# Performance work log

Hardware: AMD Instinct MI355X
Metric: run time of the kernel (lower is better)

Reference implementation:

```python
import jax, jax.numpy as jnp
import numpy as np

B, S, D, H, F, M = 4, 2048, 1024, 16, 4096, 1024
HD = D // H
EPS = 1e-6


def _rms(x, scale):
    # flax nn.RMSNorm: x * rsqrt(mean(x^2) + eps) * scale
    return x * jax.lax.rsqrt(jnp.mean(x * x, axis=-1, keepdims=True) + EPS) * scale


def setup_inputs() -> dict:
    key = jax.random.key(0)
    ks = jax.random.split(key, 40)
    w = lambda k, shape: jax.random.normal(k, shape, jnp.float32) * 0.02
    inp = {
        'x': jax.random.normal(ks[0], (B, S, D), jnp.float32),
        'mem_k': jax.random.normal(ks[1], (B, M, D), jnp.float32),
        'mem_v': jax.random.normal(ks[2], (B, M, D), jnp.float32),
        'n1': jnp.ones((D,), jnp.float32),
        'n2': jnp.ones((D,), jnp.float32),
        'wq': w(ks[3], (D, D)), 'bq': jnp.zeros((D,), jnp.float32),
        'wk': w(ks[4], (D, D)), 'bk': jnp.zeros((D,), jnp.float32),
        'wv': w(ks[5], (D, D)), 'bv': jnp.zeros((D,), jnp.float32),
        'wz': w(ks[6], (D, D)), 'bz': jnp.zeros((D,), jnp.float32),
        'wgz': w(ks[7], (D, D)), 'bgz': jnp.zeros((D,), jnp.float32),
        'wgh': w(ks[8], (D, D)), 'bgh': jnp.zeros((D,), jnp.float32),
        'wg1': w(ks[9], (D, D // 4)), 'bg1': jnp.zeros((D // 4,), jnp.float32),
        'wg2': w(ks[10], (D // 4, D)), 'bg2': jnp.full((D,), -3.0, jnp.float32),
        'wc1': w(ks[11], (D, D // 4)), 'bc1': jnp.zeros((D // 4,), jnp.float32),
        'wc2': w(ks[12], (D // 4, D)), 'bc2': jnp.zeros((D,), jnp.float32),
        'wak': w(ks[13], (D, D)), 'bak': jnp.zeros((D,), jnp.float32),
        'wav': w(ks[14], (D, D)), 'bav': jnp.zeros((D,), jnp.float32),
        'wao': w(ks[15], (D, D)), 'bao': jnp.zeros((D,), jnp.float32),
        'w1': w(ks[16], (D, F)), 'b1': jnp.zeros((F,), jnp.float32),
        'w2': w(ks[17], (F, D)), 'b2': jnp.zeros((D,), jnp.float32),
    }
    return inp


def reference(x, mem_k, mem_v, n1, n2, wq, bq, wk, bk, wv, bv, wz, bz,
              wgz, bgz, wgh, bgh, wg1, bg1, wg2, bg2, wc1, bc1, wc2, bc2,
              wak, bak, wav, bav, wao, bao, w1, b1, w2, b2):
    x_norm = _rms(x, n1)
    q = x_norm @ wq + bq
    k = x_norm @ wk + bk
    v = x_norm @ wv + bv
    z = x_norm @ wz + bz

    # decay gamma: base from z, context modulation from k
    gamma_base = jax.nn.sigmoid(jax.nn.gelu(x_norm @ wz @ jnp.zeros((0,)) if False else (z @ wg1 + bg1)) @ wg2 + bg2)
    gamma_mod = jax.nn.sigmoid(jax.nn.gelu(k @ wc1 + bc1) @ wc2 + bc2)
    gamma = jnp.clip(gamma_base * gamma_mod, 1e-6, 1.0 - 1e-6)

    gate_z_seq = z @ wgz + bgz
    h0 = jnp.zeros((x.shape[0], D), x.dtype)

    def scan_fn(h_prev, inputs):
        gz_t, z_t, g_t = inputs  # each [B, D]
        gate = jax.nn.sigmoid(gz_t + h_prev @ wgh + bgh)
        h_tilde = (1.0 - gate) * h_prev + gate * z_t
        h_t = jnp.clip(h_tilde + g_t * h_prev, -100.0, 100.0)
        return h_t, h_t

    xs = (jnp.swapaxes(gate_z_seq, 0, 1), jnp.swapaxes(z, 0, 1), jnp.swapaxes(gamma, 0, 1))
    _, h_seq_T = jax.lax.scan(scan_fn, h0, xs)  # [S, B, D]
    h_sequence = jnp.swapaxes(h_seq_T, 0, 1)  # [B, S, D]

    # MultiMemoryAttention: queries from q_input, keys/values from memory state
    qh = q.reshape(B, S, H, HD)
    kh = (mem_k @ wak + bak).reshape(B, M, H, HD)
    vh = (mem_v @ wav + bav).reshape(B, M, H, HD)
    scores = jnp.einsum('bqhd,bkhd->bhqk', qh, kh) / jnp.sqrt(jnp.float32(HD))
    attn = jax.nn.softmax(scores, axis=-1)
    mem_out = jnp.einsum('bhqk,bkhd->bqhd', attn, vh).reshape(B, S, D) @ wao + bao

    combined = h_sequence + mem_out + v * 0.1
    x_residual = x + combined  # dropout deterministic
    x_norm2 = _rms(x_residual, n2)
    h_ffn = jax.nn.gelu(x_norm2 @ w1 + b1) @ w2 + b2
    return x_residual + h_ffn
```

## Files before the change

kernel.cpp:

```cpp
#include <hip/hip_runtime.h>

namespace {

constexpr int kB = 4, kS = 2048, kD = 1024, kH = 16, kF = 4096, kM = 1024;
constexpr int kBS = kB * kS;
constexpr int kBM = kB * kM;

#define DEV __device__ __forceinline__

DEV float bf2f(unsigned short u){ unsigned int i = ((unsigned int)u) << 16; float f; __builtin_memcpy(&f, &i, 4); return f; }
DEV unsigned short f2bf(float f){ unsigned int i; __builtin_memcpy(&i, &f, 4); return (unsigned short)((i + 0x7fffu + ((i >> 16) & 1u)) >> 16); }
DEV float gelu_f(float x){ float u = 0.7978845608028654f * (x + 0.044715f * x * x * x); return 0.5f * x * (1.0f + tanhf(u)); }
DEV float sigmoid_f(float x){ return 1.0f / (1.0f + __expf(-x)); }

typedef __attribute__((ext_vector_type(8))) short bf16x8;
typedef __attribute__((ext_vector_type(4))) float f32x4;
typedef __attribute__((address_space(1))) const unsigned char gas_u8;
typedef __attribute__((address_space(3))) unsigned char las_u8;

__global__ __launch_bounds__(256) void k_transpose_bf16(const float* __restrict__ W, unsigned short* __restrict__ Wt, int K, int N){
  __shared__ float tile[32][33];
  int n0 = blockIdx.x * 32, k0 = blockIdx.y * 32;
  int tx = threadIdx.x, ty = threadIdx.y;
  for (int i = ty; i < 32; i += 8) tile[i][tx] = W[(size_t)(k0 + i) * N + n0 + tx];
  __syncthreads();
  for (int i = ty; i < 32; i += 8) Wt[(size_t)(n0 + i) * K + k0 + tx] = f2bf(tile[tx][i]);
}

__global__ __launch_bounds__(256) void k_rmsnorm(const float* __restrict__ x, const float* __restrict__ scale, unsigned short* __restrict__ out){
  int row = blockIdx.x;
  int t = threadIdx.x;
  float4 v = ((const float4*)(x + (size_t)row * kD))[t];
  float ss = v.x*v.x + v.y*v.y + v.z*v.z + v.w*v.w;
  for (int o = 32; o > 0; o >>= 1) ss += __shfl_xor(ss, o);
  __shared__ float red[4];
  int wave = t >> 6, lane = t & 63;
  if (lane == 0) red[wave] = ss;
  __syncthreads();
  float tot = red[0] + red[1] + red[2] + red[3];
  float r = rsqrtf(tot * (1.0f / kD) + 1e-6f);
  float4 s = ((const float4*)scale)[t];
  ushort4 o4;
  o4.x = f2bf(v.x * r * s.x); o4.y = f2bf(v.y * r * s.y);
  o4.z = f2bf(v.z * r * s.z); o4.w = f2bf(v.w * r * s.w);
  *(ushort4*)(out + (size_t)row * kD + t * 4) = o4;
}

__global__ __launch_bounds__(256) void k_f32_to_bf16(const float* __restrict__ in, unsigned short* __restrict__ out, int n4){
  int i = blockIdx.x * 256 + threadIdx.x;
  int stride = gridDim.x * 256;
  for (; i < n4; i += stride){
    float4 v = ((const float4*)in)[i];
    ushort4 o; o.x = f2bf(v.x); o.y = f2bf(v.y); o.z = f2bf(v.z); o.w = f2bf(v.w);
    ((ushort4*)out)[i] = o;
  }
}

__global__ __launch_bounds__(256) void k_combine(float* __restrict__ xres, const float* __restrict__ x,
                                                 const float* __restrict__ h, const unsigned short* __restrict__ v, int n4){
  int i = blockIdx.x * 256 + threadIdx.x;
  int stride = gridDim.x * 256;
  for (; i < n4; i += stride){
    float4 a = ((float4*)xres)[i];
    float4 xv = ((const float4*)x)[i];
    float4 hv = ((const float4*)h)[i];
    ushort4 vv = ((const ushort4*)v)[i];
    a.x += xv.x + hv.x + 0.1f * bf2f(vv.x);
    a.y += xv.y + hv.y + 0.1f * bf2f(vv.y);
    a.z += xv.z + hv.z + 0.1f * bf2f(vv.z);
    a.w += xv.w + hv.w + 0.1f * bf2f(vv.w);
    ((float4*)xres)[i] = a;
  }
}

template<int EPI>
__global__ __launch_bounds__(256) void gemm_kernel(
    const unsigned short* __restrict__ A, int lda,
    const unsigned short* __restrict__ Bt, int ldb,
    const float* __restrict__ bias,
    float* __restrict__ out1, unsigned short* __restrict__ out2,
    const float* __restrict__ src,
    int Mdim, int Ndim, int Kdim,
    const float* __restrict__ b_k = nullptr,
    const float* __restrict__ b_v = nullptr,
    const float* __restrict__ b_z = nullptr,
    unsigned short* __restrict__ o_k = nullptr,
    unsigned short* __restrict__ o_v = nullptr,
    unsigned short* __restrict__ o_zb = nullptr)
{
  __shared__ unsigned short As[128 * 32];
  __shared__ unsigned short Bs[128 * 32];
  const int t = threadIdx.x;
  const int wave = t >> 6, lane = t & 63;
  const int m0 = blockIdx.y * 128, n0 = blockIdx.x * 128;
  const int wr = (wave >> 1) * 64, wc = (wave & 1) * 64;
  const int lr = lane & 15, lk = lane >> 4;

  f32x4 acc[4][4];
  #pragma unroll
  for (int m = 0; m < 4; ++m)
    #pragma unroll
    for (int n = 0; n < 4; ++n) acc[m][n] = (f32x4){0.f, 0.f, 0.f, 0.f};

  const int r0 = t >> 2, s0 = (t & 3) * 8;
  const int r1 = 64 + r0;
  las_u8* lA0 = (las_u8*)(void*)(As + r0 * 32 + s0);
  las_u8* lA1 = (las_u8*)(void*)(As + r1 * 32 + s0);
  las_u8* lB0 = (las_u8*)(void*)(Bs + r0 * 32 + s0);
  las_u8* lB1 = (las_u8*)(void*)(Bs + r1 * 32 + s0);

  for (int k0 = 0; k0 < Kdim; k0 += 32){
    __syncthreads();
    __builtin_amdgcn_global_load_lds((gas_u8*)(const void*)(A  + (size_t)(m0 + r0) * lda + k0 + s0), lA0, 16, 0, 0);
    __builtin_amdgcn_global_load_lds((gas_u8*)(const void*)(A  + (size_t)(m0 + r1) * lda + k0 + s0), lA1, 16, 0, 0);
    __builtin_amdgcn_global_load_lds((gas_u8*)(const void*)(Bt + (size_t)(n0 + r0) * ldb + k0 + s0), lB0, 16, 0, 0);
    __builtin_amdgcn_global_load_lds((gas_u8*)(const void*)(Bt + (size_t)(n0 + r1) * ldb + k0 + s0), lB1, 16, 0, 0);
    __syncthreads();
    bf16x8 af[4], bfr[4];
    #pragma unroll
    for (int m = 0; m < 4; ++m) af[m] = *(const bf16x8*)(As + (wr + m * 16 + lr) * 32 + lk * 8);
    #pragma unroll
    for (int n = 0; n < 4; ++n) bfr[n] = *(const bf16x8*)(Bs + (wc + n * 16 + lr) * 32 + lk * 8);
    #pragma unroll
    for (int m = 0; m < 4; ++m)
      #pragma unroll
      for (int n = 0; n < 4; ++n)
        acc[m][n] = __builtin_amdgcn_mfma_f32_16x16x32_bf16(af[m], bfr[n], acc[m][n], 0, 0, 0);
  }

  const float* bsel = bias;
  unsigned short* osel = out2;
  int sel = 0;
  if constexpr (EPI == 8){
    sel = n0 >> 10;
    bsel = (sel == 0) ? bias : (sel == 1) ? b_k : (sel == 2) ? b_v : b_z;
    osel = (sel == 0) ? out2 : (sel == 1) ? o_k : (sel == 2) ? o_v : o_zb;
  }

  #pragma unroll
  for (int m = 0; m < 4; ++m){
    #pragma unroll
    for (int n = 0; n < 4; ++n){
      int col = n0 + wc + n * 16 + lr;
      float bv;
      if constexpr (EPI == 8) bv = bsel[col & 1023];
      else bv = bias ? bias[col] : 0.f;
      #pragma unroll
      for (int r = 0; r < 4; ++r){
        int rowg = m0 + wr + m * 16 + lk * 4 + r;
        size_t off = (size_t)rowg * Ndim + col;
        float v = acc[m][n][r] + bv;
        if constexpr (EPI == 0) out1[off] = v;
        else if constexpr (EPI == 1) out2[off] = f2bf(v);
        else if constexpr (EPI == 2) out2[off] = f2bf(gelu_f(v));
        else if constexpr (EPI == 3) out1[off] = sigmoid_f(v);
        else if constexpr (EPI == 4){ float g = out1[off] * sigmoid_f(v); out1[off] = fminf(fmaxf(g, 1e-6f), 1.0f - 1e-6f); }
        else if constexpr (EPI == 5){ out1[off] = v; out2[off] = f2bf(v); }
        else if constexpr (EPI == 6) out1[off] = src[off] + v;
        else if constexpr (EPI == 7) out1[off] += v;
        else if constexpr (EPI == 8){
          size_t off8 = (size_t)rowg * 1024 + (col & 1023);
          if (sel == 3){ out1[off8] = v; osel[off8] = f2bf(v); }
          else osel[off8] = f2bf(v);
        }
        else if constexpr (EPI == 9){
          int bb = rowg >> 10, key = rowg & 1023, hh = col >> 6, dd = col & 63;
          out2[(((size_t)bb * 16 + hh) * 64 + dd) * 1024 + key] = f2bf(v);
        }
      }
    }
  }
}

__global__ __launch_bounds__(256) void k_scan(const float* __restrict__ wgh,
                                              const float* __restrict__ gz,
                                              float* __restrict__ zh ,
                                              const float* __restrict__ gamma,
                                              const float* __restrict__ bgh,
                                              unsigned long long* __restrict__ hpub){
  __shared__ unsigned short wsl[1024 * 32];
  __shared__ float hl[1024];
  __shared__ float red[4][32];
  const int t = threadIdx.x;
  const int bid = blockIdx.x;
  const int b = bid & 3, slc = bid >> 2;
  const int colg0 = slc * 32;

  for (int idx = t; idx < 32768; idx += 256){
    int k = idx >> 5, c = idx & 31;
    wsl[idx] = f2bf(wgh[(size_t)k * 1024 + colg0 + c]);
  }
  const float bghv = (t < 32) ? bgh[colg0 + t] : 0.f;
  const int lane = t & 63, w = t >> 6;
  const int lgrp = lane >> 3;
  const int lcol = lane & 7;
  const int ibase = w * 256;
  __syncthreads();

  for (int tt = 0; tt < kS; ++tt){
    if (tt > 0){
      const unsigned want = (unsigned)(tt - 1);
      unsigned long long* pb = hpub + (((size_t)((tt - 1) & 1)) * kB + b) * 1024 + ibase + (lane << 2);
      unsigned long long pv0 = __hip_atomic_load(pb + 0, __ATOMIC_RELAXED, __HIP_MEMORY_SCOPE_AGENT);
      unsigned long long pv1 = __hip_atomic_load(pb + 1, __ATOMIC_RELAXED, __HIP_MEMORY_SCOPE_AGENT);
      unsigned long long pv2 = __hip_atomic_load(pb + 2, __ATOMIC_RELAXED, __HIP_MEMORY_SCOPE_AGENT);
      unsigned long long pv3 = __hip_atomic_load(pb + 3, __ATOMIC_RELAXED, __HIP_MEMORY_SCOPE_AGENT);
      while (true){
        bool ok = ((unsigned)(pv0 >> 32) == want) && ((unsigned)(pv1 >> 32) == want)
               && ((unsigned)(pv2 >> 32) == want) && ((unsigned)(pv3 >> 32) == want);
        if (__all(ok)) break;
        pv0 = __hip_atomic_load(pb + 0, __ATOMIC_RELAXED, __HIP_MEMORY_SCOPE_AGENT);
        pv1 = __hip_atomic_load(pb + 1, __ATOMIC_RELAXED, __HIP_MEMORY_SCOPE_AGENT);
        pv2 = __hip_atomic_load(pb + 2, __ATOMIC_RELAXED, __HIP_MEMORY_SCOPE_AGENT);
        pv3 = __hip_atomic_load(pb + 3, __ATOMIC_RELAXED, __HIP_MEMORY_SCOPE_AGENT);
      }
      int hbase = ibase + (lane << 2);
      hl[hbase + 0] = __uint_as_float((unsigned)pv0);
      hl[hbase + 1] = __uint_as_float((unsigned)pv1);
      hl[hbase + 2] = __uint_as_float((unsigned)pv2);
      hl[hbase + 3] = __uint_as_float((unsigned)pv3);
    } else {
      ((float4*)hl)[t] = make_float4(0.f, 0.f, 0.f, 0.f);
    }
    asm volatile("" ::: "memory");
    float gzv = 0.f, zv = 0.f, gv = 0.f;
    size_t inidx = 0;
    if (t < 32){
      inidx = ((size_t)b * kS + tt) * 1024 + colg0 + t;
      gzv = gz[inidx]; zv = zh[inidx]; gv = gamma[inidx];
    }

    float a0 = 0.f, a1 = 0.f, a2 = 0.f, a3 = 0.f;
    const unsigned short* wb = wsl + ibase * 32;
    #pragma unroll 4
    for (int j = 0; j < 32; ++j){
      int i = j * 8 + lgrp;
      float hv = hl[ibase + i];
      uint2 ww = *(const uint2*)(wb + i * 32 + lcol * 4);
      a0 += hv * bf2f((unsigned short)(ww.x & 0xffffu));
      a1 += hv * bf2f((unsigned short)(ww.x >> 16));
      a2 += hv * bf2f((unsigned short)(ww.y & 0xffffu));
      a3 += hv * bf2f((unsigned short)(ww.y >> 16));
    }
    for (int o = 8; o < 64; o <<= 1){
      a0 += __shfl_xor(a0, o); a1 += __shfl_xor(a1, o);
      a2 += __shfl_xor(a2, o); a3 += __shfl_xor(a3, o);
    }
    if (lane < 8){
      red[w][lane * 4 + 0] = a0; red[w][lane * 4 + 1] = a1;
      red[w][lane * 4 + 2] = a2; red[w][lane * 4 + 3] = a3;
    }
    __syncthreads();

    if (t < 32){
      float sum = red[0][t] + red[1][t] + red[2][t] + red[3][t];
      float gate = sigmoid_f(gzv + sum + bghv);
      float hp = hl[colg0 + t];
      float ht = (1.0f - gate) * hp + gate * zv + gv * hp;
      ht = fminf(fmaxf(ht, -100.0f), 100.0f);
      zh[inidx] = ht;
      unsigned long long pv = ((unsigned long long)(unsigned)tt << 32)
                            | (unsigned long long)__float_as_uint(ht);
      __hip_atomic_store(hpub + (((size_t)(tt & 1)) * kB + b) * 1024 + colg0 + t, pv,
                         __ATOMIC_RELAXED, __HIP_MEMORY_SCOPE_AGENT);
    }
    __syncthreads();
  }
}

__global__ __launch_bounds__(256) void k_attn_mfma(const unsigned short* __restrict__ q,
                                                   const unsigned short* __restrict__ kh,
                                                   const unsigned short* __restrict__ vhT,
                                                   unsigned short* __restrict__ ao){
  __shared__ unsigned short Qs[2][64][32];
  __shared__ unsigned short Ks[2][128][32];
  __shared__ unsigned short Vt[4][64][32];
  __shared__ unsigned short Ps[4][4][16][32];
  const int t = threadIdx.x;
  const int qt = blockIdx.x, h = blockIdx.y, b = blockIdx.z;
  const int lane = t & 63, w = t >> 6;
  const int lk = lane >> 4, lr = lane & 15;

  for (int i = t; i < 512; i += 256){
    int row = i >> 3, cg = (i & 7) * 8;
    *(uint4*)&Qs[cg >> 5][row][cg & 31] =
      *(const uint4*)(q + ((size_t)(b * kS + qt * 64 + row)) * kD + h * 64 + cg);
  }

  f32x4 acc_o[4];
  #pragma unroll
  for (int n = 0; n < 4; ++n) acc_o[n] = (f32x4){0.f, 0.f, 0.f, 0.f};
  float m_[4], l_[4];
  #pragma unroll
  for (int r = 0; r < 4; ++r){ m_[r] = -3e38f; l_[r] = 0.f; }

  for (int c = 0; c < 8; ++c){
    __syncthreads();
    for (int i = t; i < 1024; i += 256){
      int key = i >> 3, cg = (i & 7) * 8;
      *(uint4*)&Ks[cg >> 5][key][cg & 31] =
        *(const uint4*)(kh + ((size_t)(b * kM + c * 128 + key)) * kD + h * 64 + cg);
    }
    for (int i = t; i < 1024; i += 256){
      int d = i >> 4, kg = (i & 15) * 8;
      *(uint4*)&Vt[kg >> 5][d][kg & 31] =
        *(const uint4*)(vhT + (((size_t)(b * 16 + h)) * 64 + d) * 1024 + c * 128 + kg);
    }
    __syncthreads();

    f32x4 accs[8];
    #pragma unroll
    for (int n = 0; n < 8; ++n) accs[n] = (f32x4){0.f, 0.f, 0.f, 0.f};
    #pragma unroll
    for (int kk = 0; kk < 2; ++kk){
      bf16x8 aq = *(const bf16x8*)&Qs[kk][16 * w + lr][lk * 8];
      #pragma unroll
      for (int n = 0; n < 8; ++n){
        bf16x8 bk8 = *(const bf16x8*)&Ks[kk][16 * n + lr][lk * 8];
        accs[n] = __builtin_amdgcn_mfma_f32_16x16x32_bf16(aq, bk8, accs[n], 0, 0, 0);
      }
    }

    #pragma unroll
    for (int n = 0; n < 8; ++n)
      #pragma unroll
      for (int r = 0; r < 4; ++r) accs[n][r] *= 0.125f;
    float mnew[4], alpha[4], psum[4];
    #pragma unroll
    for (int r = 0; r < 4; ++r){
      float mx = accs[0][r];
      #pragma unroll
      for (int n = 1; n < 8; ++n) mx = fmaxf(mx, accs[n][r]);
      #pragma unroll
      for (int o = 1; o < 16; o <<= 1) mx = fmaxf(mx, __shfl_xor(mx, o));
      mnew[r] = fmaxf(m_[r], mx);
      alpha[r] = __expf(m_[r] - mnew[r]);
      m_[r] = mnew[r];
      psum[r] = 0.f;
    }
    #pragma unroll
    for (int n = 0; n < 8; ++n){
      #pragma unroll
      for (int r = 0; r < 4; ++r){
        float p = __expf(accs[n][r] - mnew[r]);
        psum[r] += p;
        Ps[w][n >> 1][lk * 4 + r][16 * (n & 1) + lr] = f2bf(p);
      }
    }
    #pragma unroll
    for (int r = 0; r < 4; ++r){
      float s = psum[r];
      #pragma unroll
      for (int o = 1; o < 16; o <<= 1) s += __shfl_xor(s, o);
      l_[r] = l_[r] * alpha[r] + s;
      #pragma unroll
      for (int n = 0; n < 4; ++n) acc_o[n][r] *= alpha[r];
    }

    #pragma unroll
    for (int kk = 0; kk < 4; ++kk){
      bf16x8 ap = *(const bf16x8*)&Ps[w][kk][lr][lk * 8];
      #pragma unroll
      for (int n = 0; n < 4; ++n){
        bf16x8 bv8 = *(const bf16x8*)&Vt[kk][16 * n + lr][lk * 8];
        acc_o[n] = __builtin_amdgcn_mfma_f32_16x16x32_bf16(ap, bv8, acc_o[n], 0, 0, 0);
      }
    }
  }

  #pragma unroll
  for (int n = 0; n < 4; ++n){
    #pragma unroll
    for (int r = 0; r < 4; ++r){
      size_t off = ((size_t)(b * kS + qt * 64 + 16 * w + lk * 4 + r)) * kD + h * 64 + 16 * n + lr;
      ao[off] = f2bf(acc_o[n][r] / l_[r]);
    }
  }
}

}

extern "C" void kernel_launch(void* const* d_in, const int* in_sizes, int n_in,
                              void* d_out, int out_size, void* d_ws, size_t ws_size,
                              hipStream_t stream){
  (void)in_sizes; (void)n_in; (void)out_size;
  const float* x    = (const float*)d_in[0];
  const float* memk = (const float*)d_in[1];
  const float* memv = (const float*)d_in[2];
  const float* n1   = (const float*)d_in[3];
  const float* n2   = (const float*)d_in[4];
  const float* wq   = (const float*)d_in[5];   const float* bq  = (const float*)d_in[6];
  const float* wk   = (const float*)d_in[7];   const float* bk  = (const float*)d_in[8];
  const float* wv   = (const float*)d_in[9];   const float* bv  = (const float*)d_in[10];
  const float* wz   = (const float*)d_in[11];  const float* bz  = (const float*)d_in[12];
  const float* wgz  = (const float*)d_in[13];  const float* bgz = (const float*)d_in[14];
  const float* wgh  = (const float*)d_in[15];  const float* bgh = (const float*)d_in[16];
  const float* wg1  = (const float*)d_in[17];  const float* bg1 = (const float*)d_in[18];
  const float* wg2  = (const float*)d_in[19];  const float* bg2 = (const float*)d_in[20];
  const float* wc1  = (const float*)d_in[21];  const float* bc1 = (const float*)d_in[22];
  const float* wc2  = (const float*)d_in[23];  const float* bc2 = (const float*)d_in[24];
  const float* wak  = (const float*)d_in[25];  const float* bak = (const float*)d_in[26];
  const float* wav  = (const float*)d_in[27];  const float* bav = (const float*)d_in[28];
  const float* wao  = (const float*)d_in[29];  const float* bao = (const float*)d_in[30];
  const float* w1   = (const float*)d_in[31];  const float* b1  = (const float*)d_in[32];
  const float* w2   = (const float*)d_in[33];  const float* b2  = (const float*)d_in[34];
  float* outp = (float*)d_out;
  char* ws = (char*)d_ws;
  const size_t MBy = 1024ull * 1024ull;
  if (ws_size < 252 * MBy) return;

  unsigned short* wq_t  = (unsigned short*)(ws + 0 * MBy);
  unsigned short* wk_t  = (unsigned short*)(ws + 2 * MBy);
  unsigned short* wv_t  = (unsigned short*)(ws + 4 * MBy);
  unsigned short* wz_t  = (unsigned short*)(ws + 6 * MBy);
  unsigned short* wgz_t = (unsigned short*)(ws + 8 * MBy);
  unsigned short* wak_t = (unsigned short*)(ws + 10 * MBy);
  unsigned short* wav_t = (unsigned short*)(ws + 12 * MBy);
  unsigned short* wao_t = (unsigned short*)(ws + 14 * MBy);
  unsigned short* wg1_t = (unsigned short*)(ws + 16 * MBy);
  unsigned short* wg2_t = (unsigned short*)(ws + 16 * MBy + 524288);
  unsigned short* wc1_t = (unsigned short*)(ws + 16 * MBy + 2 * 524288);
  unsigned short* wc2_t = (unsigned short*)(ws + 16 * MBy + 3 * 524288);
  unsigned short* w1_t  = (unsigned short*)(ws + 18 * MBy);
  unsigned short* w2_t  = (unsigned short*)(ws + 26 * MBy);
  unsigned long long* hpub = (unsigned long long*)(ws + 34 * MBy);
  unsigned short* xn    = (unsigned short*)(ws + 40 * MBy);
  unsigned short* memk_b= (unsigned short*)(ws + 40 * MBy);
  unsigned short* memv_b= (unsigned short*)(ws + 48 * MBy);
  unsigned short* ao    = (unsigned short*)(ws + 40 * MBy);
  unsigned short* qb_   = (unsigned short*)(ws + 56 * MBy);
  unsigned short* xn2   = (unsigned short*)(ws + 56 * MBy);
  unsigned short* kb_   = (unsigned short*)(ws + 72 * MBy);
  unsigned short* khb   = (unsigned short*)(ws + 72 * MBy);
  unsigned short* vhT   = (unsigned short*)(ws + 80 * MBy);
  unsigned short* vb_   = (unsigned short*)(ws + 88 * MBy);
  float*          zf    = (float*)(ws + 104 * MBy);
  unsigned short* zb_   = (unsigned short*)(ws + 136 * MBy);
  unsigned short* mid   = (unsigned short*)(ws + 136 * MBy);
  float*          gzf   = (float*)(ws + 152 * MBy);
  float*          gmf   = (float*)(ws + 184 * MBy);
  unsigned short* g1b   = (unsigned short*)(ws + 216 * MBy);
  float*          xres  = (float*)(ws + 220 * MBy);

  dim3 tb(32, 8);
  k_transpose_bf16<<<dim3(32, 32), tb, 0, stream>>>(wq,  wq_t,  1024, 1024);
  k_transpose_bf16<<<dim3(32, 32), tb, 0, stream>>>(wk,  wk_t,  1024, 1024);
  k_transpose_bf16<<<dim3(32, 32), tb, 0, stream>>>(wv,  wv_t,  1024, 1024);
  k_transpose_bf16<<<dim3(32, 32), tb, 0, stream>>>(wz,  wz_t,  1024, 1024);
  k_transpose_bf16<<<dim3(32, 32), tb, 0, stream>>>(wgz, wgz_t, 1024, 1024);
  k_transpose_bf16<<<dim3(32, 32), tb, 0, stream>>>(wak, wak_t, 1024, 1024);
  k_transpose_bf16<<<dim3(32, 32), tb, 0, stream>>>(wav, wav_t, 1024, 1024);
  k_transpose_bf16<<<dim3(32, 32), tb, 0, stream>>>(wao, wao_t, 1024, 1024);
  k_transpose_bf16<<<dim3(8, 32),  tb, 0, stream>>>(wg1, wg1_t, 1024, 256);
  k_transpose_bf16<<<dim3(32, 8),  tb, 0, stream>>>(wg2, wg2_t, 256, 1024);
  k_transpose_bf16<<<dim3(8, 32),  tb, 0, stream>>>(wc1, wc1_t, 1024, 256);
  k_transpose_bf16<<<dim3(32, 8),  tb, 0, stream>>>(wc2, wc2_t, 256, 1024);
  k_transpose_bf16<<<dim3(128, 32),tb, 0, stream>>>(w1,  w1_t,  1024, 4096);
  k_transpose_bf16<<<dim3(32, 128),tb, 0, stream>>>(w2,  w2_t,  4096, 1024);

  k_rmsnorm<<<kBS, 256, 0, stream>>>(x, n1, xn);
  gemm_kernel<8><<<dim3(32, 64), 256, 0, stream>>>(xn, 1024, wq_t, 1024, bq, zf, qb_, nullptr,
                                                   kBS, 4096, 1024, bk, bv, bz, kb_, vb_, zb_);

  gemm_kernel<0><<<dim3(8, 64), 256, 0, stream>>>(zb_, 1024, wgz_t, 1024, bgz, gzf, nullptr, nullptr, kBS, 1024, 1024);
  gemm_kernel<2><<<dim3(2, 64), 256, 0, stream>>>(zb_, 1024, wg1_t, 1024, bg1, nullptr, g1b, nullptr, kBS, 256, 1024);
  gemm_kernel<3><<<dim3(8, 64), 256, 0, stream>>>(g1b, 256, wg2_t, 256, bg2, gmf, nullptr, nullptr, kBS, 1024, 256);
  gemm_kernel<2><<<dim3(2, 64), 256, 0, stream>>>(kb_, 1024, wc1_t, 1024, bc1, nullptr, g1b, nullptr, kBS, 256, 1024);
  gemm_kernel<4><<<dim3(8, 64), 256, 0, stream>>>(g1b, 256, wc2_t, 256, bc2, gmf, nullptr, nullptr, kBS, 1024, 256);

  hipMemsetAsync(hpub, 0xFF, 65536, stream);
  k_scan<<<128, 256, 0, stream>>>(wgh, gzf, zf, gmf, bgh, hpub);

  k_f32_to_bf16<<<1024, 256, 0, stream>>>(memk, memk_b, kBM * kD / 4);
  k_f32_to_bf16<<<1024, 256, 0, stream>>>(memv, memv_b, kBM * kD / 4);
  gemm_kernel<1><<<dim3(8, 32), 256, 0, stream>>>(memk_b, 1024, wak_t, 1024, bak, nullptr, khb, nullptr, kBM, 1024, 1024);
  gemm_kernel<9><<<dim3(8, 32), 256, 0, stream>>>(memv_b, 1024, wav_t, 1024, bav, nullptr, vhT, nullptr, kBM, 1024, 1024);
  k_attn_mfma<<<dim3(32, 16, 4), 256, 0, stream>>>(qb_, khb, vhT, ao);
  gemm_kernel<0><<<dim3(8, 64), 256, 0, stream>>>(ao, 1024, wao_t, 1024, bao, xres, nullptr, nullptr, kBS, 1024, 1024);

  k_combine<<<2048, 256, 0, stream>>>(xres, x, zf, vb_, kBS * kD / 4);
  k_rmsnorm<<<kBS, 256, 0, stream>>>(xres, n2, xn2);
  gemm_kernel<2><<<dim3(16, 64), 256, 0, stream>>>(xn2, 1024, w1_t, 1024, b1, nullptr, mid, nullptr, kBS, 2048, 1024);
  gemm_kernel<6><<<dim3(8, 64), 256, 0, stream>>>(mid, 2048, w2_t, 4096, b2, outp, nullptr, xres, kBS, 1024, 2048);
  gemm_kernel<2><<<dim3(16, 64), 256, 0, stream>>>(xn2, 1024, w1_t + (size_t)2048 * 1024, 1024, b1 + 2048, nullptr, mid, nullptr, kBS, 2048, 1024);
  gemm_kernel<7><<<dim3(8, 64), 256, 0, stream>>>(mid, 2048, w2_t + 2048, 4096, nullptr, outp, nullptr, nullptr, kBS, 1024, 2048);
}
```

Baseline: 5.219 ms.

## Overlap recurrent h-state polling with partial matvec in chunked slices

In the sequential gated-recurrence kernel, each wave used to wait for all 256 of its published h values before starting the hidden-to-gate matvec. Now it polls four 64-element chunks with lane-contiguous atomic loads and accumulates the matching slice of the matvec as each chunk arrives. The inputs gz, z and gamma are also loaded earlier, right after the first chunk. The aim is to hide inter-block publication latency on the critical serial path, at the cost of more wave-level vote loops and separate polling per chunk.

```diff
diff --git a/kernel.cpp b/kernel.cpp
--- a/kernel.cpp
+++ b/kernel.cpp
@@ -198,50 +198,63 @@
   __syncthreads();
 
   for (int tt = 0; tt < kS; ++tt){
+    float a0 = 0.f, a1 = 0.f, a2 = 0.f, a3 = 0.f;
+    float gzv = 0.f, zv = 0.f, gv = 0.f;
+    size_t inidx = 0;
+    const unsigned short* wb = wsl + ibase * 32;
+
+#define MACSLICE(R) { \
+      _Pragma("unroll") \
+      for (int j = 8*(R); j < 8*(R) + 8; ++j){ \
+        int i = j * 8 + lgrp; \
+        float hv = hl[ibase + i]; \
+        uint2 ww = *(const uint2*)(wb + i * 32 + lcol * 4); \
+        a0 += hv * bf2f((unsigned short)(ww.x & 0xffffu)); \
+        a1 += hv * bf2f((unsigned short)(ww.x >> 16)); \
+        a2 += hv * bf2f((unsigned short)(ww.y & 0xffffu)); \
+        a3 += hv * bf2f((unsigned short)(ww.y >> 16)); \
+      } }
+
     if (tt > 0){
       const unsigned want = (unsigned)(tt - 1);
-      unsigned long long* pb = hpub + (((size_t)((tt - 1) & 1)) * kB + b) * 1024 + ibase + (lane << 2);
-      unsigned long long pv0 = __hip_atomic_load(pb + 0, __ATOMIC_RELAXED, __HIP_MEMORY_SCOPE_AGENT);
-      unsigned long long pv1 = __hip_atomic_load(pb + 1, __ATOMIC_RELAXED, __HIP_MEMORY_SCOPE_AGENT);
-      unsigned long long pv2 = __hip_atomic_load(pb + 2, __ATOMIC_RELAXED, __HIP_MEMORY_SCOPE_AGENT);
-      unsigned long long pv3 = __hip_atomic_load(pb + 3, __ATOMIC_RELAXED, __HIP_MEMORY_SCOPE_AGENT);
-      while (true){
-        bool ok = ((unsigned)(pv0 >> 32) == want) && ((unsigned)(pv1 >> 32) == want)
-               && ((unsigned)(pv2 >> 32) == want) && ((unsigned)(pv3 >> 32) == want);
-        if (__all(ok)) break;
+      unsigned long long* pb = hpub + (((size_t)((tt - 1) & 1)) * kB + b) * 1024 + ibase + lane;
+      unsigned long long pv0 = __hip_atomic_load(pb +   0, __ATOMIC_RELAXED, __HIP_MEMORY_SCOPE_AGENT);
+      unsigned long long pv1 = __hip_atomic_load(pb +  64, __ATOMIC_RELAXED, __HIP_MEMORY_SCOPE_AGENT);
+      unsigned long long pv2 = __hip_atomic_load(pb + 128, __ATOMIC_RELAXED, __HIP_MEMORY_SCOPE_AGENT);
+      unsigned long long pv3 = __hip_atomic_load(pb + 192, __ATOMIC_RELAXED, __HIP_MEMORY_SCOPE_AGENT);
+      while (__any((unsigned)(pv0 >> 32) != want))
         pv0 = __hip_atomic_load(pb + 0, __ATOMIC_RELAXED, __HIP_MEMORY_SCOPE_AGENT);
-        pv1 = __hip_atomic_load(pb + 1, __ATOMIC_RELAXED, __HIP_MEMORY_SCOPE_AGENT);
-        pv2 = __hip_atomic_load(pb + 2, __ATOMIC_RELAXED, __HIP_MEMORY_SCOPE_AGENT);
-        pv3 = __hip_atomic_load(pb + 3, __ATOMIC_RELAXED, __HIP_MEMORY_SCOPE_AGENT);
+      hl[ibase + lane] = __uint_as_float((unsigned)pv0);
+      asm volatile("" ::: "memory");
+      if (t < 32){
+        inidx = ((size_t)b * kS + tt) * 1024 + colg0 + t;
+        gzv = gz[inidx]; zv = zh[inidx]; gv = gamma[inidx];
       }
-      int hbase = ibase + (lane << 2);
-      hl[hbase + 0] = __uint_as_float((unsigned)pv0);
-      hl[hbase + 1] = __uint_as_float((unsigned)pv1);
-      hl[hbase + 2] = __uint_as_float((unsigned)pv2);
-      hl[hbase + 3] = __uint_as_float((unsigned)pv3);
+      asm volatile("" ::: "memory");
+      MACSLICE(0)
+      while (__any((unsigned)(pv1 >> 32) != want))
+        pv1 = __hip_atomic_load(pb + 64, __ATOMIC_RELAXED, __HIP_MEMORY_SCOPE_AGENT);
+      hl[ibase + 64 + lane] = __uint_as_float((unsigned)pv1);
+      MACSLICE(1)
+      while (__any((unsigned)(pv2 >> 32) != want))
+        pv2 = __hip_atomic_load(pb + 128, __ATOMIC_RELAXED, __HIP_MEMORY_SCOPE_AGENT);
+      hl[ibase + 128 + lane] = __uint_as_float((unsigned)pv2);
+      MACSLICE(2)
+      while (__any((unsigned)(pv3 >> 32) != want))
+        pv3 = __hip_atomic_load(pb + 192, __ATOMIC_RELAXED, __HIP_MEMORY_SCOPE_AGENT);
+      hl[ibase + 192 + lane] = __uint_as_float((unsigned)pv3);
+      MACSLICE(3)
     } else {
-      ((float4*)hl)[t] = make_float4(0.f, 0.f, 0.f, 0.f);
-    }
-    asm volatile("" ::: "memory");
-    float gzv = 0.f, zv = 0.f, gv = 0.f;
-    size_t inidx = 0;
-    if (t < 32){
-      inidx = ((size_t)b * kS + tt) * 1024 + colg0 + t;
-      gzv = gz[inidx]; zv = zh[inidx]; gv = gamma[inidx];
-    }
-
-    float a0 = 0.f, a1 = 0.f, a2 = 0.f, a3 = 0.f;
-    const unsigned short* wb = wsl + ibase * 32;
-    #pragma unroll 4
-    for (int j = 0; j < 32; ++j){
-      int i = j * 8 + lgrp;
-      float hv = hl[ibase + i];
-      uint2 ww = *(const uint2*)(wb + i * 32 + lcol * 4);
-      a0 += hv * bf2f((unsigned short)(ww.x & 0xffffu));
-      a1 += hv * bf2f((unsigned short)(ww.x >> 16));
-      a2 += hv * bf2f((unsigned short)(ww.y & 0xffffu));
-      a3 += hv * bf2f((unsigned short)(ww.y >> 16));
-    }
+      hl[ibase + lane] = 0.f; hl[ibase + 64 + lane] = 0.f;
+      hl[ibase + 128 + lane] = 0.f; hl[ibase + 192 + lane] = 0.f;
+      if (t < 32){
+        inidx = ((size_t)b * kS) * 1024 + colg0 + t;
+        gzv = gz[inidx]; zv = zh[inidx]; gv = gamma[inidx];
+      }
+      MACSLICE(0) MACSLICE(1) MACSLICE(2) MACSLICE(3)
+    }
+#undef MACSLICE
+
     for (int o = 8; o < 64; o <<= 1){
       a0 += __shfl_xor(a0, o); a1 += __shfl_xor(a1, o);
       a2 += __shfl_xor(a2, o); a3 += __shfl_xor(a3, o);
```

Result: slower. 5.596 ms (+7.2%).
